# Kernel tuning notes

Hardware: AMD Instinct MI355X
Metric: run time of the kernel (lower is better)

The kernel has to match this reference:

```python
import jax, jax.numpy as jnp
import numpy as np

N_Q = 8  # number of residual quantization levels


def setup_inputs() -> dict:
    key = jax.random.key(0)
    k1, k2 = jax.random.split(key)
    hidden_states = jax.random.normal(k1, (8192, 128), dtype=jnp.float32)
    codebooks = jax.random.normal(k2, (N_Q, 256, 128), dtype=jnp.float32)
    return {"hidden_states": hidden_states, "codebooks": codebooks}


def reference(hidden_states, codebooks):
    """Residual VQ encode: per level, nearest codebook entry by L2, subtract, accumulate.

    hidden_states: [N, D]; codebooks: [n_q, bins, D].
    Returns (codes [n_q, N] int, quantized [N, D]).
    """
    residual = hidden_states
    quantized = jnp.zeros_like(hidden_states)
    codes = []
    for i in range(N_Q):  # small fixed loop over structurally distinct levels
        codebook = codebooks[i]  # [bins, D]
        # squared L2 distance, same math as the original broadcasted form
        dist = jnp.sum((residual[:, None, :] - codebook[None, :, :]) ** 2, axis=-1)  # [N, bins]
        idx = jnp.argmin(dist, axis=-1)  # [N]
        chosen = codebook[idx]  # [N, D]
        quantized = quantized + chosen
        residual = residual - chosen
        codes.append(idx)
    return jnp.stack(codes, axis=0), quantized
```

## Files before the change

kernel.cpp:

```cpp
#include <hip/hip_runtime.h>

#define NQ 8
#define BINS 256
#define D 128
#define RPB 32
#define THREADS 1024
#define RSTRIDE 132
#define FREG 520

typedef short s8v __attribute__((ext_vector_type(8)));
typedef short s4v __attribute__((ext_vector_type(4)));
typedef float f4v __attribute__((ext_vector_type(4)));

static __device__ __forceinline__ unsigned short bf16_rtne(float x) {
    unsigned u = __float_as_uint(x);
    unsigned r = (u + 0x7fffu + ((u >> 16) & 1u)) >> 16;
    return (unsigned short)r;
}
static __device__ __forceinline__ float bf16_to_f(unsigned short h) {
    return __uint_as_float(((unsigned)h) << 16);
}
struct Split3 { short h, m, l; };
static __device__ __forceinline__ Split3 split3(float x) {
    Split3 s;
    unsigned short hb = bf16_rtne(x);
    float r1 = x - bf16_to_f(hb);
    unsigned short mb = bf16_rtne(r1);
    unsigned short lb = bf16_rtne(r1 - bf16_to_f(mb));
    s.h = (short)hb; s.m = (short)mb; s.l = (short)lb;
    return s;
}
static __device__ __forceinline__ unsigned long long u64min(unsigned long long a, unsigned long long b) {
    return a < b ? a : b;
}
static __device__ __forceinline__ unsigned dpp_row_min16(unsigned v) {
    unsigned t;
    t = (unsigned)__builtin_amdgcn_update_dpp(0, (int)v, 0xB1,  0xF, 0xF, true); v = v < t ? v : t;
    t = (unsigned)__builtin_amdgcn_update_dpp(0, (int)v, 0x4E,  0xF, 0xF, true); v = v < t ? v : t;
    t = (unsigned)__builtin_amdgcn_update_dpp(0, (int)v, 0x124, 0xF, 0xF, true); v = v < t ? v : t;
    t = (unsigned)__builtin_amdgcn_update_dpp(0, (int)v, 0x128, 0xF, 0xF, true); v = v < t ? v : t;
    return v;
}

__global__ __launch_bounds__(256) void rvq_prep(
    const float* __restrict__ cb, short* __restrict__ cb_hi,
    short* __restrict__ cb_mid, short* __restrict__ cb_lo,
    float* __restrict__ c2)
{
    __shared__ float st[16 * RSTRIDE];
    const int L = blockIdx.x >> 4;
    const int o = blockIdx.x & 15;
    const int t = threadIdx.x;

    const float4* src = (const float4*)(cb + ((size_t)L * BINS + o * 16) * D);
    #pragma unroll
    for (int i = 0; i < 2; ++i) {
        int f4 = i * 256 + t;
        int row = f4 >> 5, c4 = f4 & 31;
        float4 v = src[f4];
        float* d = &st[row * RSTRIDE + c4 * 4];
        d[0] = v.x; d[1] = v.y; d[2] = v.z; d[3] = v.w;
    }
    __syncthreads();

    const int bin = t >> 4;
    const int kc  = t & 15;
    const float* p = &st[bin * RSTRIDE + kc * 8];
    s8v h8, m8, l8;
    float s = 0.f;
    #pragma unroll
    for (int j = 0; j < 8; ++j) {
        float x = p[j];
        Split3 sp = split3(x);
        h8[j] = sp.h; m8[j] = sp.m; l8[j] = sp.l;
        s = fmaf(x, x, s);
    }
    int idx = (L * 16 + kc) * BINS + (o * 16 + bin);
    ((s8v*)cb_hi)[idx]  = h8;
    ((s8v*)cb_mid)[idx] = m8;
    ((s8v*)cb_lo)[idx]  = l8;
    s += __shfl_xor(s, 1, 64);
    s += __shfl_xor(s, 2, 64);
    s += __shfl_xor(s, 4, 64);
    s += __shfl_xor(s, 8, 64);
    if (kc == 0) c2[L * BINS + o * 16 + bin] = s;
}

static __device__ __forceinline__ void frag_store4(
    const float* rres, short* ah, short* am, short* al, int rr_, int g8, int half)
{
    s4v h4, m4, l4;
    #pragma unroll
    for (int j = 0; j < 4; ++j) {
        Split3 sp = split3(rres[j]);
        h4[j] = sp.h; m4[j] = sp.m; l4[j] = sp.l;
    }
    int q = g8 & 3;
    int reg = (rr_ >> 4) * 4 + (g8 >> 2);
    int idx16 = q * 16 + (((rr_ & 15) + 4 * q) & 15);
    int off = reg * FREG + idx16 * 8 + half * 4;
    *(s4v*)&ah[off] = h4;
    *(s4v*)&am[off] = m4;
    *(s4v*)&al[off] = l4;
}

static __device__ __forceinline__ void issue_b(
    int lv, int bin, int quad,
    const s8v* __restrict__ bhp, const s8v* __restrict__ bmp, const s8v* __restrict__ blp,
    const float* __restrict__ c2p,
    s8v bh[4], s8v bm[4], s8v bl[4], float& c2v)
{
    c2v = c2p[lv * BINS + bin];
    #pragma unroll
    for (int ks = 0; ks < 4; ++ks) {
        int idx = (lv * 16 + ks * 4 + quad) * BINS + bin;
        bh[ks] = bhp[idx];
        bm[ks] = bmp[idx];
        bl[ks] = blp[idx];
    }
}

__global__ __launch_bounds__(THREADS) void rvq_kernel(
    const float* __restrict__ hidden,
    const float* __restrict__ cb_f32,
    const short* __restrict__ cb_hi,
    const short* __restrict__ cb_mid,
    const short* __restrict__ cb_lo,
    const float* __restrict__ c2p,
    float* __restrict__ out_codes,
    float* __restrict__ out_quant,
    int N)
{
    __shared__ short ah[8 * FREG];
    __shared__ short am[8 * FREG];
    __shared__ short al[8 * FREG];
    __shared__ __align__(16) unsigned long long redw[RPB][18];

    const int t = threadIdx.x;
    const int w = t >> 6;
    const int l = t & 63;
    const int quad = l >> 4;
    const int m = l & 15;
    const int row0 = blockIdx.x * RPB;
    const int woff = w * 16;
    const int bin = woff + m;
    const int rr_ = t >> 5;
    const int gd  = t & 31;
    const int g8  = gd >> 1;
    const int half = gd & 1;

    float rres[4];
    {
        const float4* hp = (const float4*)(hidden + (size_t)(row0 + rr_) * D + gd * 4);
        float4 v = *hp;
        rres[0] = v.x; rres[1] = v.y; rres[2] = v.z; rres[3] = v.w;
    }
    frag_store4(rres, ah, am, al, rr_, g8, half);

    const s8v* bhp = (const s8v*)cb_hi;
    const s8v* bmp = (const s8v*)cb_mid;
    const s8v* blp = (const s8v*)cb_lo;

    s8v bh[4], bm[4], bl[4];
    float c2v;
    issue_b(0, bin, quad, bhp, bmp, blp, c2p, bh, bm, bl, c2v);

    for (int level = 0; level < NQ; ++level) {
        __syncthreads();

        unsigned ucand[2][4];
        const int idx16 = quad * 16 + ((m + 4 * quad) & 15);
        #pragma unroll
        for (int mt = 0; mt < 2; ++mt) {
            s8v afh[4], afm[4], afl[4];
            #pragma unroll
            for (int ks = 0; ks < 4; ++ks) {
                int off = (mt * 4 + ks) * FREG + idx16 * 8;
                afh[ks] = *(const s8v*)&ah[off];
                afm[ks] = *(const s8v*)&am[off];
                afl[ks] = *(const s8v*)&al[off];
            }
            f4v a0 = {0.f, 0.f, 0.f, 0.f};
            f4v a1 = {0.f, 0.f, 0.f, 0.f};
            f4v a2 = {0.f, 0.f, 0.f, 0.f};
            #pragma unroll
            for (int ks = 0; ks < 4; ++ks) {
                a0 = __builtin_amdgcn_mfma_f32_16x16x32_bf16(afh[ks], bh[ks], a0, 0, 0, 0);
                a1 = __builtin_amdgcn_mfma_f32_16x16x32_bf16(afh[ks], bm[ks], a1, 0, 0, 0);
                a1 = __builtin_amdgcn_mfma_f32_16x16x32_bf16(afm[ks], bh[ks], a1, 0, 0, 0);
                a2 = __builtin_amdgcn_mfma_f32_16x16x32_bf16(afm[ks], bm[ks], a2, 0, 0, 0);
                a2 = __builtin_amdgcn_mfma_f32_16x16x32_bf16(afh[ks], bl[ks], a2, 0, 0, 0);
                a2 = __builtin_amdgcn_mfma_f32_16x16x32_bf16(afl[ks], bh[ks], a2, 0, 0, 0);
            }
            #pragma unroll
            for (int i = 0; i < 4; ++i) {
                float dot = a0[i] + (a1[i] + a2[i]);
                float k = fmaf(-2.f, dot, c2v);
                unsigned u = __float_as_uint(k);
                u = (u & 0x80000000u) ? ~u : (u | 0x80000000u);
                ucand[mt][i] = u;
            }
        }

        #pragma unroll
        for (int mt = 0; mt < 2; ++mt)
            #pragma unroll
            for (int i = 0; i < 4; ++i) {
                unsigned v = ucand[mt][i];
                unsigned r = dpp_row_min16(v);
                unsigned long long mk = __ballot(v == r);
                unsigned grp = (unsigned)(mk >> (quad * 16)) & 0xffffu;
                int bmin = woff + __builtin_ctz(grp);
                if (m == 0)
                    redw[mt * 16 + quad * 4 + i][w] =
                        ((unsigned long long)r << 32) | (unsigned)bmin;
            }
        __syncthreads();

        if (level + 1 < NQ)
            issue_b(level + 1, bin, quad, bhp, bmp, blp, c2p, bh, bm, bl, c2v);

        unsigned long long mn;
        {
            const ulonglong2* rp = (const ulonglong2*)&redw[rr_][0];
            ulonglong2 p0 = rp[0], p1 = rp[1], p2 = rp[2], p3 = rp[3];
            ulonglong2 p4 = rp[4], p5 = rp[5], p6 = rp[6], p7 = rp[7];
            unsigned long long a = u64min(u64min(u64min(p0.x, p0.y), u64min(p1.x, p1.y)),
                                          u64min(u64min(p2.x, p2.y), u64min(p3.x, p3.y)));
            unsigned long long b = u64min(u64min(u64min(p4.x, p4.y), u64min(p5.x, p5.y)),
                                          u64min(u64min(p6.x, p6.y), u64min(p7.x, p7.y)));
            mn = u64min(a, b);
        }
        const int wb = (int)(mn & 0xffffffffull);
        if (gd == 0)
            out_codes[(size_t)level * N + row0 + rr_] = (float)wb;

        {
            const float4* cp = (const float4*)(cb_f32 + ((size_t)level * BINS + wb) * D + gd * 4);
            float4 c = *cp;
            rres[0] -= c.x; rres[1] -= c.y; rres[2] -= c.z; rres[3] -= c.w;
        }
        if (level + 1 < NQ)
            frag_store4(rres, ah, am, al, rr_, g8, half);
    }

    {
        const float4* hp = (const float4*)(hidden + (size_t)(row0 + rr_) * D + gd * 4);
        float4 v = *hp;
        float4 q;
        q.x = v.x - rres[0]; q.y = v.y - rres[1]; q.z = v.z - rres[2]; q.w = v.w - rres[3];
        *(float4*)(out_quant + (size_t)(row0 + rr_) * D + gd * 4) = q;
    }
}

extern "C" void kernel_launch(void* const* d_in, const int* in_sizes, int n_in,
                              void* d_out, int out_size, void* d_ws, size_t ws_size,
                              hipStream_t stream) {
    const float* hidden    = (const float*)d_in[0];
    const float* codebooks = (const float*)d_in[1];
    float* out = (float*)d_out;
    const int N = in_sizes[0] / D;
    float* out_codes = out;
    float* out_quant = out + (size_t)NQ * N;

    char* ws = (char*)d_ws;
    short* cb_hi  = (short*)ws;
    short* cb_mid = (short*)(ws +  512 * 1024);
    short* cb_lo  = (short*)(ws + 1024 * 1024);
    float* c2     = (float*)(ws + 1536 * 1024);

    rvq_prep<<<dim3(NQ * 16), 256, 0, stream>>>(codebooks, cb_hi, cb_mid, cb_lo, c2);
    rvq_kernel<<<dim3(N / RPB), THREADS, 0, stream>>>(
        hidden, codebooks, cb_hi, cb_mid, cb_lo, c2, out_codes, out_quant, N);
}
```

Before: 106.7 us.

## Halve rows per block, give each wave two bin tiles with in-loop B reload

Blocks shrink from 32 rows and 1024 threads to 16 rows and 512 threads, so 8 waves cover 256 bins with 32 bins each. Each wave reuses one A fragment across two 16-bin N-tiles and reloads the B fragments for the second tile midway through the level. The argmin merges the two tiles with two ballots, and the cross-wave reduction shrinks to 8 entries. This doubles the grid and adds a launch-bounds occupancy hint to improve latency hiding and occupancy, at the cost of re-reading codebook B fragments twice per level per block and splitting codebook reuse over fewer rows.

New measurement: 129.7 us. 21.5% more time.

```diff
diff --git a/kernel.cpp b/kernel.cpp
--- a/kernel.cpp
+++ b/kernel.cpp
@@ -3,8 +3,8 @@
 #define NQ 8
 #define BINS 256
 #define D 128
-#define RPB 32
-#define THREADS 1024
+#define RPB 16
+#define THREADS 512
 #define RSTRIDE 132
 #define FREG 520
 
@@ -96,8 +96,8 @@
         h4[j] = sp.h; m4[j] = sp.m; l4[j] = sp.l;
     }
     int q = g8 & 3;
-    int reg = (rr_ >> 4) * 4 + (g8 >> 2);
-    int idx16 = q * 16 + (((rr_ & 15) + 4 * q) & 15);
+    int reg = g8 >> 2;
+    int idx16 = q * 16 + ((rr_ + 4 * q) & 15);
     int off = reg * FREG + idx16 * 8 + half * 4;
     *(s4v*)&ah[off] = h4;
     *(s4v*)&am[off] = m4;
@@ -120,7 +120,7 @@
     }
 }
 
-__global__ __launch_bounds__(THREADS) void rvq_kernel(
+__global__ __launch_bounds__(THREADS, 4) void rvq_kernel(
     const float* __restrict__ hidden,
     const float* __restrict__ cb_f32,
     const short* __restrict__ cb_hi,
@@ -131,10 +131,10 @@
     float* __restrict__ out_quant,
     int N)
 {
-    __shared__ short ah[8 * FREG];
-    __shared__ short am[8 * FREG];
-    __shared__ short al[8 * FREG];
-    __shared__ __align__(16) unsigned long long redw[RPB][18];
+    __shared__ __align__(16) short ah[4 * FREG];
+    __shared__ __align__(16) short am[4 * FREG];
+    __shared__ __align__(16) short al[4 * FREG];
+    __shared__ __align__(16) unsigned long long redw[RPB][10];
 
     const int t = threadIdx.x;
     const int w = t >> 6;
@@ -142,16 +142,16 @@
     const int quad = l >> 4;
     const int m = l & 15;
     const int row0 = blockIdx.x * RPB;
-    const int woff = w * 16;
-    const int bin = woff + m;
-    const int rr_ = t >> 5;
-    const int gd  = t & 31;
-    const int g8  = gd >> 1;
+    const int woff = w * 32;
+    const int rr_  = t >> 5;
+    const int gd   = t & 31;
+    const int g8   = gd >> 1;
     const int half = gd & 1;
+    const int dbase = g8 * 8 + half * 4;
 
     float rres[4];
     {
-        const float4* hp = (const float4*)(hidden + (size_t)(row0 + rr_) * D + gd * 4);
+        const float4* hp = (const float4*)(hidden + (size_t)(row0 + rr_) * D + dbase);
         float4 v = *hp;
         rres[0] = v.x; rres[1] = v.y; rres[2] = v.z; rres[3] = v.w;
     }
@@ -163,23 +163,26 @@
 
     s8v bh[4], bm[4], bl[4];
     float c2v;
-    issue_b(0, bin, quad, bhp, bmp, blp, c2p, bh, bm, bl, c2v);
+    issue_b(0, woff + m, quad, bhp, bmp, blp, c2p, bh, bm, bl, c2v);
 
     for (int level = 0; level < NQ; ++level) {
         __syncthreads();
 
-        unsigned ucand[2][4];
-        const int idx16 = quad * 16 + ((m + 4 * quad) & 15);
-        #pragma unroll
-        for (int mt = 0; mt < 2; ++mt) {
-            s8v afh[4], afm[4], afl[4];
+        s8v afh[4], afm[4], afl[4];
+        {
+            const int idx16 = quad * 16 + ((m + 4 * quad) & 15);
             #pragma unroll
             for (int ks = 0; ks < 4; ++ks) {
-                int off = (mt * 4 + ks) * FREG + idx16 * 8;
+                int off = ks * FREG + idx16 * 8;
                 afh[ks] = *(const s8v*)&ah[off];
                 afm[ks] = *(const s8v*)&am[off];
                 afl[ks] = *(const s8v*)&al[off];
             }
+        }
+
+        unsigned vkey[2][4];
+        #pragma unroll
+        for (int nt = 0; nt < 2; ++nt) {
             f4v a0 = {0.f, 0.f, 0.f, 0.f};
             f4v a1 = {0.f, 0.f, 0.f, 0.f};
             f4v a2 = {0.f, 0.f, 0.f, 0.f};
@@ -192,51 +195,50 @@
                 a2 = __builtin_amdgcn_mfma_f32_16x16x32_bf16(afh[ks], bl[ks], a2, 0, 0, 0);
                 a2 = __builtin_amdgcn_mfma_f32_16x16x32_bf16(afl[ks], bh[ks], a2, 0, 0, 0);
             }
+            float c2cur = c2v;
+            if (nt == 0)
+                issue_b(level, woff + 16 + m, quad, bhp, bmp, blp, c2p, bh, bm, bl, c2v);
             #pragma unroll
             for (int i = 0; i < 4; ++i) {
                 float dot = a0[i] + (a1[i] + a2[i]);
-                float k = fmaf(-2.f, dot, c2v);
+                float k = fmaf(-2.f, dot, c2cur);
                 unsigned u = __float_as_uint(k);
                 u = (u & 0x80000000u) ? ~u : (u | 0x80000000u);
-                ucand[mt][i] = u;
+                vkey[nt][i] = u;
             }
         }
 
         #pragma unroll
-        for (int mt = 0; mt < 2; ++mt)
-            #pragma unroll
-            for (int i = 0; i < 4; ++i) {
-                unsigned v = ucand[mt][i];
-                unsigned r = dpp_row_min16(v);
-                unsigned long long mk = __ballot(v == r);
-                unsigned grp = (unsigned)(mk >> (quad * 16)) & 0xffffu;
-                int bmin = woff + __builtin_ctz(grp);
-                if (m == 0)
-                    redw[mt * 16 + quad * 4 + i][w] =
-                        ((unsigned long long)r << 32) | (unsigned)bmin;
-            }
+        for (int i = 0; i < 4; ++i) {
+            unsigned v0 = vkey[0][i], v1 = vkey[1][i];
+            unsigned vm = v0 < v1 ? v0 : v1;
+            unsigned r  = dpp_row_min16(vm);
+            unsigned long long mk0 = __ballot(v0 == r);
+            unsigned long long mk1 = __ballot(v1 == r);
+            unsigned gg0 = (unsigned)(mk0 >> (quad * 16)) & 0xffffu;
+            unsigned gg1 = (unsigned)(mk1 >> (quad * 16)) & 0xffffu;
+            int bmin = woff + (gg0 ? __builtin_ctz(gg0) : 16 + __builtin_ctz(gg1));
+            if (m == 0)
+                redw[quad * 4 + i][w] = ((unsigned long long)r << 32) | (unsigned)bmin;
+        }
         __syncthreads();
 
         if (level + 1 < NQ)
-            issue_b(level + 1, bin, quad, bhp, bmp, blp, c2p, bh, bm, bl, c2v);
+            issue_b(level + 1, woff + m, quad, bhp, bmp, blp, c2p, bh, bm, bl, c2v);
 
         unsigned long long mn;
         {
             const ulonglong2* rp = (const ulonglong2*)&redw[rr_][0];
             ulonglong2 p0 = rp[0], p1 = rp[1], p2 = rp[2], p3 = rp[3];
-            ulonglong2 p4 = rp[4], p5 = rp[5], p6 = rp[6], p7 = rp[7];
-            unsigned long long a = u64min(u64min(u64min(p0.x, p0.y), u64min(p1.x, p1.y)),
-                                          u64min(u64min(p2.x, p2.y), u64min(p3.x, p3.y)));
-            unsigned long long b = u64min(u64min(u64min(p4.x, p4.y), u64min(p5.x, p5.y)),
-                                          u64min(u64min(p6.x, p6.y), u64min(p7.x, p7.y)));
-            mn = u64min(a, b);
+            mn = u64min(u64min(u64min(p0.x, p0.y), u64min(p1.x, p1.y)),
+                        u64min(u64min(p2.x, p2.y), u64min(p3.x, p3.y)));
         }
         const int wb = (int)(mn & 0xffffffffull);
         if (gd == 0)
             out_codes[(size_t)level * N + row0 + rr_] = (float)wb;
 
         {
-            const float4* cp = (const float4*)(cb_f32 + ((size_t)level * BINS + wb) * D + gd * 4);
+            const float4* cp = (const float4*)(cb_f32 + ((size_t)level * BINS + wb) * D + dbase);
             float4 c = *cp;
             rres[0] -= c.x; rres[1] -= c.y; rres[2] -= c.z; rres[3] -= c.w;
         }
@@ -245,11 +247,11 @@
     }
 
     {
-        const float4* hp = (const float4*)(hidden + (size_t)(row0 + rr_) * D + gd * 4);
+        const float4* hp = (const float4*)(hidden + (size_t)(row0 + rr_) * D + dbase);
         float4 v = *hp;
         float4 q;
         q.x = v.x - rres[0]; q.y = v.y - rres[1]; q.z = v.z - rres[2]; q.w = v.w - rres[3];
-        *(float4*)(out_quant + (size_t)(row0 + rr_) * D + gd * 4) = q;
+        *(float4*)(out_quant + (size_t)(row0 + rr_) * D + dbase) = q;
     }
 }
 
```
